# Optimization experiments

Measured on AMD Instinct MI355X. Metric: run time of the kernel, lower is better.

## Reference

```python
import jax, jax.numpy as jnp
import numpy as np

B, S, D, T = 64, 512, 768, 64


def setup_inputs() -> dict:
    key = jax.random.key(0)
    k1, k2, k3 = jax.random.split(key, 3)
    x = jax.random.normal(k1, (B, S, D), dtype=jnp.float32)
    W = jax.random.normal(k2, (T, D), dtype=jnp.float32) * 0.02
    b = jnp.zeros((T,), dtype=jnp.float32)
    transitions = jax.random.uniform(k3, (T, T), dtype=jnp.float32, minval=-0.1, maxval=0.1)
    return {"x": x, "W": W, "b": b, "transitions": transitions}


def reference(x, W, b, transitions):
    # emissions: [B,S,T] -> [S,B,T]
    em = jnp.einsum('bsd,td->bst', x, W) + b
    em = em.transpose(1, 0, 2)

    # Viterbi forward: max-plus scan over time, collecting argmax backpointers
    def step(score, em_t):
        # score: [B,T] (prev tag), em_t: [B,T] (cur tag)
        s = score[:, :, None] + transitions[None, :, :] + em_t[:, None, :]  # [B,Tprev,Tcur]
        return jnp.max(s, axis=1), jnp.argmax(s, axis=1)

    final_score, history = jax.lax.scan(step, em[0], em[1:])  # history: [S-1,B,T]

    # Backtrack (vectorized over batch) with a reverse scan
    best = jnp.argmax(final_score, axis=-1)  # [B]

    def back(nxt, idx_t):
        prev = jnp.take_along_axis(idx_t, nxt[:, None], axis=1)[:, 0]  # [B]
        return prev, prev

    _, prev_tags = jax.lax.scan(back, best, history, reverse=True)  # [S-1,B], tags for t=0..S-2
    tags = jnp.concatenate([prev_tags, best[None, :]], axis=0)  # [S,B]
    return tags.T.astype(jnp.int32)  # [B,S]
```

## Files before the change

kernel.cpp:

```cpp
#include <hip/hip_runtime.h>

#define SS 512
#define DD 768
#define TT 64

typedef __attribute__((ext_vector_type(2))) float f32x2;

__device__ __forceinline__ f32x2 vmax2(f32x2 a, f32x2 b) {
    return __builtin_elementwise_max(a, b);
}

__global__ __launch_bounds__(256) void emis_gemm(
    const float* __restrict__ X, const float* __restrict__ W,
    const float* __restrict__ bias, float* __restrict__ em)
{
    __shared__ __align__(16) float Xs[16][68];
    __shared__ __align__(16) float Ws[16][68];

    const int tid = threadIdx.x;
    const int m0  = blockIdx.x * 64;
    const int tm  = tid >> 4;
    const int tn  = tid & 15;
    const int lr  = tid >> 2;
    const int lk  = tid & 3;

    float acc[4][4];
#pragma unroll
    for (int i = 0; i < 4; i++)
#pragma unroll
        for (int j = 0; j < 4; j++) acc[i][j] = 0.f;

    float4 xr, wr;
    xr = *(const float4*)&X[(size_t)(m0 + lr) * DD + lk * 4];
    wr = *(const float4*)&W[(size_t)lr * DD + lk * 4];

    for (int t = 0; t < 48; t++) {
        Xs[lk * 4 + 0][lr] = xr.x;  Xs[lk * 4 + 1][lr] = xr.y;
        Xs[lk * 4 + 2][lr] = xr.z;  Xs[lk * 4 + 3][lr] = xr.w;
        Ws[lk * 4 + 0][lr] = wr.x;  Ws[lk * 4 + 1][lr] = wr.y;
        Ws[lk * 4 + 2][lr] = wr.z;  Ws[lk * 4 + 3][lr] = wr.w;
        __syncthreads();

        if (t < 47) {
            const int k0 = (t + 1) * 16;
            xr = *(const float4*)&X[(size_t)(m0 + lr) * DD + k0 + lk * 4];
            wr = *(const float4*)&W[(size_t)lr * DD + k0 + lk * 4];
        }

#pragma unroll
        for (int k = 0; k < 16; k++) {
            float a[4], bv[4];
            *(float4*)&a[0]  = *(const float4*)&Xs[k][tm * 4];
            *(float4*)&bv[0] = *(const float4*)&Ws[k][tn * 4];
#pragma unroll
            for (int i = 0; i < 4; i++)
#pragma unroll
                for (int j = 0; j < 4; j++)
                    acc[i][j] = fmaf(a[i], bv[j], acc[i][j]);
        }
        __syncthreads();
    }

    const float4 bv4 = *(const float4*)&bias[tn * 4];
#pragma unroll
    for (int i = 0; i < 4; i++) {
        const size_t row = (size_t)(m0 + tm * 4 + i);
        float4 o;
        o.x = acc[i][0] + bv4.x;  o.y = acc[i][1] + bv4.y;
        o.z = acc[i][2] + bv4.z;  o.w = acc[i][3] + bv4.w;
        *(float4*)&em[row * TT + tn * 4] = o;
    }
}

__global__ __launch_bounds__(64)
__attribute__((amdgpu_waves_per_eu(1, 1)))
void viterbi_fwd(
    const float* __restrict__ em, const float* __restrict__ trans,
    float* __restrict__ scoreHist, int* __restrict__ bestTag)
{
    __shared__ __align__(16) float sc_lds[TT];
    __shared__ __align__(16) float tr_lds[4096];

    const int b    = blockIdx.x;
    const int lane = threadIdx.x;
    const float* emb = em + (size_t)b * SS * TT;
    float* sh = scoreHist + (size_t)b * SS * TT;

    {
        float4* dst = (float4*)tr_lds;
        const float4* src = (const float4*)trans;
#pragma unroll
        for (int i = 0; i < 16; i++) dst[lane + i * 64] = src[lane + i * 64];
    }
    __syncthreads();

    f32x2 tpk[32];
#pragma unroll
    for (int j = 0; j < 32; j++) {
        tpk[j].x = tr_lds[(2 * j) * TT + lane];
        tpk[j].y = tr_lds[(2 * j + 1) * TT + lane];
    }

    const float em0 = emb[lane];
    sc_lds[lane] = em0;
    sh[lane] = em0;
    float sc = em0;

    float er0 = emb[1 * TT + lane];
    float er1 = emb[2 * TT + lane];
    float er2 = emb[3 * TT + lane];
    float er3 = emb[4 * TT + lane];

    float4 sq[16];
    {
        const float4* sb = (const float4*)sc_lds;
#pragma unroll
        for (int i = 0; i < 16; i++) sq[i] = sb[i];
    }

    auto step = [&](int s, float em_v) {
        const f32x2* sq2 = (const f32x2*)sq;
        f32x2 pk[32];
#pragma unroll
        for (int j = 0; j < 32; j++) pk[j] = sq2[j] + tpk[j];

#pragma unroll
        for (int m = 16; m >= 1; m >>= 1)
#pragma unroll
            for (int j = 0; j < 16; j++) {
                if (j < m) pk[j] = vmax2(pk[j], pk[j + m]);
            }
        sc = fmaxf(pk[0].x, pk[0].y) + em_v;

        sc_lds[lane] = sc;
        {
            const float4* sb = (const float4*)sc_lds;
#pragma unroll
            for (int i = 0; i < 16; i++) sq[i] = sb[i];
        }
        sh[s * TT + lane] = sc;
    };

    for (int sb = 1; sb <= 505; sb += 4) {
        step(sb + 0, er0);  er0 = emb[(sb + 4) * TT + lane];
        step(sb + 1, er1);  er1 = emb[(sb + 5) * TT + lane];
        step(sb + 2, er2);  er2 = emb[(sb + 6) * TT + lane];
        step(sb + 3, er3);  er3 = emb[((sb + 7) <= 511 ? (sb + 7) : 511) * TT + lane];
    }
    step(509, er0);
    step(510, er1);
    step(511, er2);

    float fv = sc;
    int   fa = lane;
#pragma unroll
    for (int m = 1; m <= 32; m <<= 1) {
        const float vo = __shfl_xor(fv, m, 64);
        const int   ao = __shfl_xor(fa, m, 64);
        if (vo > fv || (vo == fv && ao < fa)) { fv = vo; fa = ao; }
    }
    if (lane == 0) bestTag[b] = fa;
}

__global__ __launch_bounds__(256) void bp_kernel(
    const float* __restrict__ scoreHist, const float* __restrict__ em,
    const float* __restrict__ trans, unsigned char* __restrict__ hist8)
{
    __shared__ __align__(16) float tr_lds[4096];
    const int tid = threadIdx.x;
    {
        const float4* src = (const float4*)trans;
        float4* dst = (float4*)tr_lds;
        for (int i = tid; i < 1024; i += 256) dst[i] = src[i];
    }
    __syncthreads();

    const int wv   = tid >> 6;
    const int lane = tid & 63;
    const int g    = blockIdx.x * 4 + wv;
    const int b    = g / 511;
    const int s    = 1 + (g % 511);

    const f32x2* sb2 = (const f32x2*)(scoreHist + ((size_t)b * SS + (s - 1)) * TT);
    const float em_v = em[((size_t)b * SS + s) * TT + lane];
    const float sh_v = scoreHist[((size_t)b * SS + s) * TT + lane];

    f32x2 tpk[32];
#pragma unroll
    for (int j = 0; j < 32; j++) {
        tpk[j].x = tr_lds[(2 * j) * TT + lane];
        tpk[j].y = tr_lds[(2 * j + 1) * TT + lane];
    }

    f32x2 em2; em2.x = em_v; em2.y = em_v;
    f32x2 v2[32];
#pragma unroll
    for (int j = 0; j < 32; j++) {
        f32x2 cand = sb2[j] + tpk[j];
        v2[j] = cand + em2;
    }

    int idx = 63;
#pragma unroll
    for (int j = 31; j >= 0; j--) {
        idx = (v2[j].y == sh_v) ? 2 * j + 1 : idx;
        idx = (v2[j].x == sh_v) ? 2 * j     : idx;
    }

    hist8[((size_t)b * SS + s) * TT + lane] = (unsigned char)idx;
}

__global__ __launch_bounds__(64) void backtrack(
    const unsigned char* __restrict__ hist8, const int* __restrict__ bestTag,
    int* __restrict__ out)
{
    __shared__ int tags[SS];

    const int b    = blockIdx.x;
    const int lane = threadIdx.x;
    const unsigned char* h8 = hist8 + (size_t)b * SS * TT;

    int tag = bestTag[b];
    if (lane == 0) tags[511] = tag;

    int r0 = h8[511 * TT + lane];
    int r1 = h8[510 * TT + lane];
    int r2 = h8[509 * TT + lane];
    int r3 = h8[508 * TT + lane];

    for (int sb = 511; sb >= 11; sb -= 4) {
        tag = __builtin_amdgcn_readlane(r0, tag);
        if (lane == 0) tags[sb - 1] = tag;
        r0 = h8[(sb - 4) * TT + lane];
        tag = __builtin_amdgcn_readlane(r1, tag);
        if (lane == 0) tags[sb - 2] = tag;
        r1 = h8[(sb - 5) * TT + lane];
        tag = __builtin_amdgcn_readlane(r2, tag);
        if (lane == 0) tags[sb - 3] = tag;
        r2 = h8[(sb - 6) * TT + lane];
        tag = __builtin_amdgcn_readlane(r3, tag);
        if (lane == 0) tags[sb - 4] = tag;
        r3 = h8[(sb - 7) * TT + lane];
    }
    tag = __builtin_amdgcn_readlane(r0, tag);  if (lane == 0) tags[6] = tag;
    tag = __builtin_amdgcn_readlane(r1, tag);  if (lane == 0) tags[5] = tag;
    tag = __builtin_amdgcn_readlane(r2, tag);  if (lane == 0) tags[4] = tag;
    tag = __builtin_amdgcn_readlane(r3, tag);  if (lane == 0) tags[3] = tag;
    int q0 = h8[3 * TT + lane];
    int q1 = h8[2 * TT + lane];
    int q2 = h8[1 * TT + lane];
    tag = __builtin_amdgcn_readlane(q0, tag);  if (lane == 0) tags[2] = tag;
    tag = __builtin_amdgcn_readlane(q1, tag);  if (lane == 0) tags[1] = tag;
    tag = __builtin_amdgcn_readlane(q2, tag);  if (lane == 0) tags[0] = tag;

    __syncthreads();
#pragma unroll
    for (int s = 0; s < 8; s++)
        out[(size_t)b * SS + s * 64 + lane] = tags[s * 64 + lane];
}

extern "C" void kernel_launch(void* const* d_in, const int* in_sizes, int n_in,
                              void* d_out, int out_size, void* d_ws, size_t ws_size,
                              hipStream_t stream)
{
    const float* X     = (const float*)d_in[0];
    const float* W     = (const float*)d_in[1];
    const float* bias  = (const float*)d_in[2];
    const float* trans = (const float*)d_in[3];
    int* out = (int*)d_out;

    char* ws = (char*)d_ws;
    float*         em        = (float*)ws;
    float*         scoreHist = (float*)(ws + 8388608);
    unsigned char* hist8     = (unsigned char*)(ws + 16777216);
    int*           bestTag   = (int*)(ws + 18874368);

    emis_gemm<<<dim3(512), dim3(256), 0, stream>>>(X, W, bias, em);
    viterbi_fwd<<<dim3(64), dim3(64), 0, stream>>>(em, trans, scoreHist, bestTag);
    bp_kernel<<<dim3(8176), dim3(256), 0, stream>>>(scoreHist, em, trans, hist8);
    backtrack<<<dim3(64), dim3(64), 0, stream>>>(hist8, bestTag, out);
}
```

Before: 227.4 us.

## Fuse emission GEMM into Viterbi kernel with producer waves double-buffering chunks

Merges the emission GEMM and the Viterbi forward scan into one kernel of 64 blocks, one per batch element. Four producer waves compute 64-row emission chunks into a double-buffered LDS tile while a fifth wave runs the serial max-plus recurrence on the previous chunk. This removes a kernel launch and the serial wave's global-memory emission reads, and hides the GEMM behind the recurrence. The cost is that the GEMM now runs on only 64 CUs, and the producer waves share a CU with the latency-critical scan wave.

```diff
diff --git a/kernel.cpp b/kernel.cpp
--- a/kernel.cpp
+++ b/kernel.cpp
@@ -10,156 +10,171 @@
     return __builtin_elementwise_max(a, b);
 }
 
-__global__ __launch_bounds__(256) void emis_gemm(
+__global__ __launch_bounds__(320)
+__attribute__((amdgpu_waves_per_eu(1, 2)))
+void fused_gemm_viterbi(
     const float* __restrict__ X, const float* __restrict__ W,
-    const float* __restrict__ bias, float* __restrict__ em)
-{
-    __shared__ __align__(16) float Xs[16][68];
-    __shared__ __align__(16) float Ws[16][68];
-
-    const int tid = threadIdx.x;
-    const int m0  = blockIdx.x * 64;
-    const int tm  = tid >> 4;
-    const int tn  = tid & 15;
-    const int lr  = tid >> 2;
-    const int lk  = tid & 3;
-
-    float acc[4][4];
-#pragma unroll
-    for (int i = 0; i < 4; i++)
-#pragma unroll
-        for (int j = 0; j < 4; j++) acc[i][j] = 0.f;
-
-    float4 xr, wr;
-    xr = *(const float4*)&X[(size_t)(m0 + lr) * DD + lk * 4];
-    wr = *(const float4*)&W[(size_t)lr * DD + lk * 4];
-
-    for (int t = 0; t < 48; t++) {
-        Xs[lk * 4 + 0][lr] = xr.x;  Xs[lk * 4 + 1][lr] = xr.y;
-        Xs[lk * 4 + 2][lr] = xr.z;  Xs[lk * 4 + 3][lr] = xr.w;
-        Ws[lk * 4 + 0][lr] = wr.x;  Ws[lk * 4 + 1][lr] = wr.y;
-        Ws[lk * 4 + 2][lr] = wr.z;  Ws[lk * 4 + 3][lr] = wr.w;
-        __syncthreads();
-
-        if (t < 47) {
-            const int k0 = (t + 1) * 16;
-            xr = *(const float4*)&X[(size_t)(m0 + lr) * DD + k0 + lk * 4];
-            wr = *(const float4*)&W[(size_t)lr * DD + k0 + lk * 4];
-        }
-
-#pragma unroll
-        for (int k = 0; k < 16; k++) {
-            float a[4], bv[4];
-            *(float4*)&a[0]  = *(const float4*)&Xs[k][tm * 4];
-            *(float4*)&bv[0] = *(const float4*)&Ws[k][tn * 4];
-#pragma unroll
-            for (int i = 0; i < 4; i++)
-#pragma unroll
-                for (int j = 0; j < 4; j++)
-                    acc[i][j] = fmaf(a[i], bv[j], acc[i][j]);
-        }
-        __syncthreads();
-    }
-
-    const float4 bv4 = *(const float4*)&bias[tn * 4];
-#pragma unroll
-    for (int i = 0; i < 4; i++) {
-        const size_t row = (size_t)(m0 + tm * 4 + i);
-        float4 o;
-        o.x = acc[i][0] + bv4.x;  o.y = acc[i][1] + bv4.y;
-        o.z = acc[i][2] + bv4.z;  o.w = acc[i][3] + bv4.w;
-        *(float4*)&em[row * TT + tn * 4] = o;
-    }
-}
-
-__global__ __launch_bounds__(64)
-__attribute__((amdgpu_waves_per_eu(1, 1)))
-void viterbi_fwd(
-    const float* __restrict__ em, const float* __restrict__ trans,
-    float* __restrict__ scoreHist, int* __restrict__ bestTag)
-{
+    const float* __restrict__ bias, const float* __restrict__ trans,
+    float* __restrict__ em, float* __restrict__ scoreHist,
+    int* __restrict__ bestTag)
+{
+    __shared__ __align__(16) float em_lds[2][64][TT];
+    __shared__ __align__(16) float tr_lds[4096];
     __shared__ __align__(16) float sc_lds[TT];
-    __shared__ __align__(16) float tr_lds[4096];
+    __shared__ __align__(16) float Xs[4][16][20];
+    __shared__ __align__(16) float Ws[4][16][64];
 
     const int b    = blockIdx.x;
-    const int lane = threadIdx.x;
-    const float* emb = em + (size_t)b * SS * TT;
-    float* sh = scoreHist + (size_t)b * SS * TT;
-
-    {
+    const int tid  = threadIdx.x;
+    const int wid  = tid >> 6;
+    const int lane = tid & 63;
+
+    float* emg = em + (size_t)b * SS * TT;
+    float* sh  = scoreHist + (size_t)b * SS * TT;
+
+    const int rgrp = lane >> 4;
+    const int cgrp = lane & 15;
+    const int xrow = lane >> 2;
+    const int xkq  = lane & 3;
+    float4 bv4;
+    if (wid < 4) bv4 = *(const float4*)&bias[cgrp * 4];
+
+    auto produce = [&](int ct, int nbuf) {
+        const float4* X4 = (const float4*)X;
+        const float4* W4 = (const float4*)W;
+        const int rowbase = b * SS + ct * 64 + wid * 16;
+
+        float acc[4][4];
+#pragma unroll
+        for (int i = 0; i < 4; i++)
+#pragma unroll
+            for (int j = 0; j < 4; j++) acc[i][j] = 0.f;
+
+        float4 xr = X4[(size_t)(rowbase + xrow) * 192 + xkq];
+        float4 w0 = W4[(size_t)lane * 192 + 0];
+        float4 w1 = W4[(size_t)lane * 192 + 1];
+        float4 w2 = W4[(size_t)lane * 192 + 2];
+        float4 w3 = W4[(size_t)lane * 192 + 3];
+
+        for (int kt = 0; kt < 48; kt++) {
+            Xs[wid][xkq * 4 + 0][xrow] = xr.x;
+            Xs[wid][xkq * 4 + 1][xrow] = xr.y;
+            Xs[wid][xkq * 4 + 2][xrow] = xr.z;
+            Xs[wid][xkq * 4 + 3][xrow] = xr.w;
+            Ws[wid][ 0][lane] = w0.x;  Ws[wid][ 1][lane] = w0.y;
+            Ws[wid][ 2][lane] = w0.z;  Ws[wid][ 3][lane] = w0.w;
+            Ws[wid][ 4][lane] = w1.x;  Ws[wid][ 5][lane] = w1.y;
+            Ws[wid][ 6][lane] = w1.z;  Ws[wid][ 7][lane] = w1.w;
+            Ws[wid][ 8][lane] = w2.x;  Ws[wid][ 9][lane] = w2.y;
+            Ws[wid][10][lane] = w2.z;  Ws[wid][11][lane] = w2.w;
+            Ws[wid][12][lane] = w3.x;  Ws[wid][13][lane] = w3.y;
+            Ws[wid][14][lane] = w3.z;  Ws[wid][15][lane] = w3.w;
+
+            if (kt < 47) {
+                xr = X4[(size_t)(rowbase + xrow) * 192 + (kt + 1) * 4 + xkq];
+                w0 = W4[(size_t)lane * 192 + (kt + 1) * 4 + 0];
+                w1 = W4[(size_t)lane * 192 + (kt + 1) * 4 + 1];
+                w2 = W4[(size_t)lane * 192 + (kt + 1) * 4 + 2];
+                w3 = W4[(size_t)lane * 192 + (kt + 1) * 4 + 3];
+            }
+
+#pragma unroll
+            for (int k = 0; k < 16; k++) {
+                float a[4], bvv[4];
+                *(float4*)&a[0]   = *(const float4*)&Xs[wid][k][rgrp * 4];
+                *(float4*)&bvv[0] = *(const float4*)&Ws[wid][k][cgrp * 4];
+#pragma unroll
+                for (int i = 0; i < 4; i++)
+#pragma unroll
+                    for (int j = 0; j < 4; j++)
+                        acc[i][j] = fmaf(a[i], bvv[j], acc[i][j]);
+            }
+        }
+
+#pragma unroll
+        for (int i = 0; i < 4; i++) {
+            const int rl = wid * 16 + rgrp * 4 + i;
+            float4 o;
+            o.x = acc[i][0] + bv4.x;  o.y = acc[i][1] + bv4.y;
+            o.z = acc[i][2] + bv4.z;  o.w = acc[i][3] + bv4.w;
+            *(float4*)&em_lds[nbuf][rl][cgrp * 4] = o;
+            *(float4*)&emg[(size_t)(ct * 64 + rl) * TT + cgrp * 4] = o;
+        }
+    };
+
+    f32x2 tpk[32];
+    if (wid == 4) {
         float4* dst = (float4*)tr_lds;
         const float4* src = (const float4*)trans;
 #pragma unroll
         for (int i = 0; i < 16; i++) dst[lane + i * 64] = src[lane + i * 64];
+#pragma unroll
+        for (int j = 0; j < 32; j++) {
+            tpk[j].x = tr_lds[(2 * j) * TT + lane];
+            tpk[j].y = tr_lds[(2 * j + 1) * TT + lane];
+        }
+    } else {
+        produce(0, 0);
     }
     __syncthreads();
 
-    f32x2 tpk[32];
-#pragma unroll
-    for (int j = 0; j < 32; j++) {
-        tpk[j].x = tr_lds[(2 * j) * TT + lane];
-        tpk[j].y = tr_lds[(2 * j + 1) * TT + lane];
-    }
-
-    const float em0 = emb[lane];
-    sc_lds[lane] = em0;
-    sh[lane] = em0;
-    float sc = em0;
-
-    float er0 = emb[1 * TT + lane];
-    float er1 = emb[2 * TT + lane];
-    float er2 = emb[3 * TT + lane];
-    float er3 = emb[4 * TT + lane];
-
+    float sc = 0.f;
     float4 sq[16];
-    {
+    if (wid == 4) {
+        sc = em_lds[0][0][lane];
+        sc_lds[lane] = sc;
+        sh[lane] = sc;
         const float4* sb = (const float4*)sc_lds;
 #pragma unroll
         for (int i = 0; i < 16; i++) sq[i] = sb[i];
     }
 
-    auto step = [&](int s, float em_v) {
-        const f32x2* sq2 = (const f32x2*)sq;
-        f32x2 pk[32];
-#pragma unroll
-        for (int j = 0; j < 32; j++) pk[j] = sq2[j] + tpk[j];
-
-#pragma unroll
-        for (int m = 16; m >= 1; m >>= 1)
-#pragma unroll
-            for (int j = 0; j < 16; j++) {
-                if (j < m) pk[j] = vmax2(pk[j], pk[j + m]);
+    int buf = 0;
+    for (int cn = 0; cn < 8; cn++) {
+        if (wid == 4) {
+            const int s0 = cn * 64;
+            const int sb_ = (cn == 0) ? 1 : s0;
+#pragma unroll 4
+            for (int s = sb_; s < s0 + 64; s++) {
+                const float em_v = em_lds[buf][s - s0][lane];
+                const f32x2* sq2 = (const f32x2*)sq;
+                f32x2 pk[32];
+#pragma unroll
+                for (int j = 0; j < 32; j++) pk[j] = sq2[j] + tpk[j];
+#pragma unroll
+                for (int m = 16; m >= 1; m >>= 1)
+#pragma unroll
+                    for (int j = 0; j < 16; j++) {
+                        if (j < m) pk[j] = vmax2(pk[j], pk[j + m]);
+                    }
+                sc = fmaxf(pk[0].x, pk[0].y) + em_v;
+
+                sc_lds[lane] = sc;
+                {
+                    const float4* sb = (const float4*)sc_lds;
+#pragma unroll
+                    for (int i = 0; i < 16; i++) sq[i] = sb[i];
+                }
+                sh[(size_t)s * TT + lane] = sc;
             }
-        sc = fmaxf(pk[0].x, pk[0].y) + em_v;
-
-        sc_lds[lane] = sc;
-        {
-            const float4* sb = (const float4*)sc_lds;
-#pragma unroll
-            for (int i = 0; i < 16; i++) sq[i] = sb[i];
-        }
-        sh[s * TT + lane] = sc;
-    };
-
-    for (int sb = 1; sb <= 505; sb += 4) {
-        step(sb + 0, er0);  er0 = emb[(sb + 4) * TT + lane];
-        step(sb + 1, er1);  er1 = emb[(sb + 5) * TT + lane];
-        step(sb + 2, er2);  er2 = emb[(sb + 6) * TT + lane];
-        step(sb + 3, er3);  er3 = emb[((sb + 7) <= 511 ? (sb + 7) : 511) * TT + lane];
-    }
-    step(509, er0);
-    step(510, er1);
-    step(511, er2);
-
-    float fv = sc;
-    int   fa = lane;
-#pragma unroll
-    for (int m = 1; m <= 32; m <<= 1) {
-        const float vo = __shfl_xor(fv, m, 64);
-        const int   ao = __shfl_xor(fa, m, 64);
-        if (vo > fv || (vo == fv && ao < fa)) { fv = vo; fa = ao; }
-    }
-    if (lane == 0) bestTag[b] = fa;
+        } else if (cn < 7) {
+            produce(cn + 1, buf ^ 1);
+        }
+        __syncthreads();
+        buf ^= 1;
+    }
+
+    if (wid == 4) {
+        float fv = sc;
+        int   fa = lane;
+#pragma unroll
+        for (int m = 1; m <= 32; m <<= 1) {
+            const float vo = __shfl_xor(fv, m, 64);
+            const int   ao = __shfl_xor(fa, m, 64);
+            if (vo > fv || (vo == fv && ao < fa)) { fv = vo; fa = ao; }
+        }
+        if (lane == 0) bestTag[b] = fa;
+    }
 }
 
 __global__ __launch_bounds__(256) void bp_kernel(
@@ -275,8 +290,8 @@
     unsigned char* hist8     = (unsigned char*)(ws + 16777216);
     int*           bestTag   = (int*)(ws + 18874368);
 
-    emis_gemm<<<dim3(512), dim3(256), 0, stream>>>(X, W, bias, em);
-    viterbi_fwd<<<dim3(64), dim3(64), 0, stream>>>(em, trans, scoreHist, bestTag);
+    fused_gemm_viterbi<<<dim3(64), dim3(320), 0, stream>>>(
+        X, W, bias, trans, em, scoreHist, bestTag);
     bp_kernel<<<dim3(8176), dim3(256), 0, stream>>>(scoreHist, em, trans, hist8);
     backtrack<<<dim3(64), dim3(64), 0, stream>>>(hist8, bestTag, out);
 }
```

Result: slower. 545.1 us (+139.7%).

## Fuse backpointer recovery into Viterbi forward kernel with LDS double-buffered score history

Applied to the files above, without the earlier changes.

Merges the forward scan and backpointer kernels into one 320-thread block per batch. Wave 0 runs the serial max-plus recurrence and writes 64-step score chunks into a double-buffered LDS history. Four helper waves meanwhile recompute argmax backpointers for the previous chunk and write hist8. This removes the global scoreHist round trip and a kernel launch, overlapping backpointer work with the serial scan. The cost is a block-wide barrier every 64 steps, and the helper waves compete with the critical-path wave for issue slots.

```diff
diff --git a/kernel.cpp b/kernel.cpp
--- a/kernel.cpp
+++ b/kernel.cpp
@@ -72,21 +72,24 @@
     }
 }
 
-__global__ __launch_bounds__(64)
-__attribute__((amdgpu_waves_per_eu(1, 1)))
-void viterbi_fwd(
+__global__ __launch_bounds__(320)
+__attribute__((amdgpu_waves_per_eu(1, 2)))
+void viterbi_fused(
     const float* __restrict__ em, const float* __restrict__ trans,
-    float* __restrict__ scoreHist, int* __restrict__ bestTag)
-{
+    unsigned char* __restrict__ hist8, int* __restrict__ bestTag)
+{
+    __shared__ __align__(16) float tr_lds[4096];
     __shared__ __align__(16) float sc_lds[TT];
-    __shared__ __align__(16) float tr_lds[4096];
+    __shared__ __align__(16) float shist[2][65][TT];
 
     const int b    = blockIdx.x;
-    const int lane = threadIdx.x;
+    const int tid  = threadIdx.x;
+    const int wid  = tid >> 6;
+    const int lane = tid & 63;
     const float* emb = em + (size_t)b * SS * TT;
-    float* sh = scoreHist + (size_t)b * SS * TT;
-
-    {
+    unsigned char* hb = hist8 + (size_t)b * SS * TT;
+
+    if (wid == 0) {
         float4* dst = (float4*)tr_lds;
         const float4* src = (const float4*)trans;
 #pragma unroll
@@ -101,29 +104,29 @@
         tpk[j].y = tr_lds[(2 * j + 1) * TT + lane];
     }
 
-    const float em0 = emb[lane];
-    sc_lds[lane] = em0;
-    sh[lane] = em0;
-    float sc = em0;
-
-    float er0 = emb[1 * TT + lane];
-    float er1 = emb[2 * TT + lane];
-    float er2 = emb[3 * TT + lane];
-    float er3 = emb[4 * TT + lane];
-
+    float sc = 0.f;
     float4 sq[16];
-    {
+    float er0 = 0.f, er1 = 0.f, er2 = 0.f, er3 = 0.f;
+    if (wid == 0) {
+        const float em0 = emb[lane];
+        sc = em0;
+        sc_lds[lane] = em0;
+        shist[0][1][lane] = em0;
+        er0 = emb[1 * TT + lane];
+        er1 = emb[2 * TT + lane];
+        er2 = emb[3 * TT + lane];
+        er3 = emb[4 * TT + lane];
         const float4* sb = (const float4*)sc_lds;
 #pragma unroll
         for (int i = 0; i < 16; i++) sq[i] = sb[i];
     }
+    __syncthreads();
 
     auto step = [&](int s, float em_v) {
         const f32x2* sq2 = (const f32x2*)sq;
         f32x2 pk[32];
 #pragma unroll
         for (int j = 0; j < 32; j++) pk[j] = sq2[j] + tpk[j];
-
 #pragma unroll
         for (int m = 16; m >= 1; m >>= 1)
 #pragma unroll
@@ -138,76 +141,80 @@
 #pragma unroll
             for (int i = 0; i < 16; i++) sq[i] = sb[i];
         }
-        sh[s * TT + lane] = sc;
+        shist[(s >> 6) & 1][(s & 63) + 1][lane] = sc;
     };
 
-    for (int sb = 1; sb <= 505; sb += 4) {
-        step(sb + 0, er0);  er0 = emb[(sb + 4) * TT + lane];
-        step(sb + 1, er1);  er1 = emb[(sb + 5) * TT + lane];
-        step(sb + 2, er2);  er2 = emb[(sb + 6) * TT + lane];
-        step(sb + 3, er3);  er3 = emb[((sb + 7) <= 511 ? (sb + 7) : 511) * TT + lane];
-    }
-    step(509, er0);
-    step(510, er1);
-    step(511, er2);
-
-    float fv = sc;
-    int   fa = lane;
-#pragma unroll
-    for (int m = 1; m <= 32; m <<= 1) {
-        const float vo = __shfl_xor(fv, m, 64);
-        const int   ao = __shfl_xor(fa, m, 64);
-        if (vo > fv || (vo == fv && ao < fa)) { fv = vo; fa = ao; }
-    }
-    if (lane == 0) bestTag[b] = fa;
-}
-
-__global__ __launch_bounds__(256) void bp_kernel(
-    const float* __restrict__ scoreHist, const float* __restrict__ em,
-    const float* __restrict__ trans, unsigned char* __restrict__ hist8)
-{
-    __shared__ __align__(16) float tr_lds[4096];
-    const int tid = threadIdx.x;
-    {
-        const float4* src = (const float4*)trans;
-        float4* dst = (float4*)tr_lds;
-        for (int i = tid; i < 1024; i += 256) dst[i] = src[i];
-    }
-    __syncthreads();
-
-    const int wv   = tid >> 6;
-    const int lane = tid & 63;
-    const int g    = blockIdx.x * 4 + wv;
-    const int b    = g / 511;
-    const int s    = 1 + (g % 511);
-
-    const f32x2* sb2 = (const f32x2*)(scoreHist + ((size_t)b * SS + (s - 1)) * TT);
-    const float em_v = em[((size_t)b * SS + s) * TT + lane];
-    const float sh_v = scoreHist[((size_t)b * SS + s) * TT + lane];
-
-    f32x2 tpk[32];
-#pragma unroll
-    for (int j = 0; j < 32; j++) {
-        tpk[j].x = tr_lds[(2 * j) * TT + lane];
-        tpk[j].y = tr_lds[(2 * j + 1) * TT + lane];
-    }
-
-    f32x2 em2; em2.x = em_v; em2.y = em_v;
-    f32x2 v2[32];
-#pragma unroll
-    for (int j = 0; j < 32; j++) {
-        f32x2 cand = sb2[j] + tpk[j];
-        v2[j] = cand + em2;
-    }
-
-    int idx = 63;
-#pragma unroll
-    for (int j = 31; j >= 0; j--) {
-        idx = (v2[j].y == sh_v) ? 2 * j + 1 : idx;
-        idx = (v2[j].x == sh_v) ? 2 * j     : idx;
-    }
-
-    hist8[((size_t)b * SS + s) * TT + lane] = (unsigned char)idx;
+    auto bp_chunk = [&](int cc) {
+        const int buf = cc & 1;
+        for (int k = 0; k < 16; ++k) {
+            const int sl = (wid - 1) + 4 * k;
+            const int s  = cc * 64 + sl;
+            if (s == 0) continue;
+            const f32x2* sb2 = (const f32x2*)&shist[buf][sl][0];
+            const float em_v = emb[(size_t)s * TT + lane];
+            const float sh_v = shist[buf][sl + 1][lane];
+            f32x2 em2; em2.x = em_v; em2.y = em_v;
+            f32x2 v2[32];
+#pragma unroll
+            for (int j = 0; j < 32; j++) {
+                f32x2 cand = sb2[j] + tpk[j];
+                v2[j] = cand + em2;
+            }
+            int idx = 63;
+#pragma unroll
+            for (int j = 31; j >= 0; j--) {
+                idx = (v2[j].y == sh_v) ? 2 * j + 1 : idx;
+                idx = (v2[j].x == sh_v) ? 2 * j     : idx;
+            }
+            hb[(size_t)s * TT + lane] = (unsigned char)idx;
+        }
+    };
+
+    for (int c = 0; c < 8; ++c) {
+        if (wid == 0) {
+            if (c > 0) shist[c & 1][0][lane] = sc;
+            if (c == 0) {
+                step(1, er0);  er0 = emb[5 * TT + lane];
+                step(2, er1);  er1 = emb[6 * TT + lane];
+                step(3, er2);  er2 = emb[7 * TT + lane];
+                for (int sb = 4; sb <= 60; sb += 4) {
+                    step(sb + 0, er3);  er3 = emb[(sb + 4) * TT + lane];
+                    step(sb + 1, er0);  er0 = emb[(sb + 5) * TT + lane];
+                    step(sb + 2, er1);  er1 = emb[(sb + 6) * TT + lane];
+                    step(sb + 3, er2);  er2 = emb[(sb + 7) * TT + lane];
+                }
+            } else {
+                for (int q = 0; q < 16; ++q) {
+                    const int sb = c * 64 + q * 4;
+                    const int p4 = (sb + 4 <= 511) ? sb + 4 : 511;
+                    const int p5 = (sb + 5 <= 511) ? sb + 5 : 511;
+                    const int p6 = (sb + 6 <= 511) ? sb + 6 : 511;
+                    const int p7 = (sb + 7 <= 511) ? sb + 7 : 511;
+                    step(sb + 0, er3);  er3 = emb[p4 * TT + lane];
+                    step(sb + 1, er0);  er0 = emb[p5 * TT + lane];
+                    step(sb + 2, er1);  er1 = emb[p6 * TT + lane];
+                    step(sb + 3, er2);  er2 = emb[p7 * TT + lane];
+                }
+            }
+        } else if (c > 0) {
+            bp_chunk(c - 1);
+        }
+        __syncthreads();
+    }
+
+    if (wid == 0) {
+        float fv = sc;
+        int   fa = lane;
+#pragma unroll
+        for (int m = 1; m <= 32; m <<= 1) {
+            const float vo = __shfl_xor(fv, m, 64);
+            const int   ao = __shfl_xor(fa, m, 64);
+            if (vo > fv || (vo == fv && ao < fa)) { fv = vo; fa = ao; }
+        }
+        if (lane == 0) bestTag[b] = fa;
+    } else {
+        bp_chunk(7);
+    }
 }
 
 __global__ __launch_bounds__(64) void backtrack(
@@ -270,13 +277,11 @@
     int* out = (int*)d_out;
 
     char* ws = (char*)d_ws;
-    float*         em        = (float*)ws;
-    float*         scoreHist = (float*)(ws + 8388608);
-    unsigned char* hist8     = (unsigned char*)(ws + 16777216);
-    int*           bestTag   = (int*)(ws + 18874368);
+    float*         em      = (float*)ws;
+    unsigned char* hist8   = (unsigned char*)(ws + 8388608);
+    int*           bestTag = (int*)(ws + 10485760);
 
     emis_gemm<<<dim3(512), dim3(256), 0, stream>>>(X, W, bias, em);
-    viterbi_fwd<<<dim3(64), dim3(64), 0, stream>>>(em, trans, scoreHist, bestTag);
-    bp_kernel<<<dim3(8176), dim3(256), 0, stream>>>(scoreHist, em, trans, hist8);
+    viterbi_fused<<<dim3(64), dim3(320), 0, stream>>>(em, trans, hist8, bestTag);
     backtrack<<<dim3(64), dim3(64), 0, stream>>>(hist8, bestTag, out);
 }
```

New measurement: 246.4 us. 8.4% more time.

## Replace LDS-tiled emission GEMM with per-wave register GEMM over transposed W

Applied to the files above, without the earlier changes.

Adds a small kernel that transposes W into workspace so each lane owns one tag column. The emission GEMM drops its shared-memory tiles and barriers: each wave computes 16 rows by 64 tags, prefetching W values into registers and reading X rows with uniform float4 loads. This removes LDS traffic and syncs. In exchange, each wave reads 16 X rows straight from global memory through the cache, and an extra kernel launch is added.

```diff
diff --git a/kernel.cpp b/kernel.cpp
--- a/kernel.cpp
+++ b/kernel.cpp
@@ -10,66 +10,53 @@
     return __builtin_elementwise_max(a, b);
 }
 
+__global__ __launch_bounds__(256) void transpose_w(
+    const float* __restrict__ W, float* __restrict__ WT)
+{
+    const int idx = blockIdx.x * 256 + threadIdx.x;
+    WT[idx] = W[(idx & 63) * DD + (idx >> 6)];
+}
+
 __global__ __launch_bounds__(256) void emis_gemm(
-    const float* __restrict__ X, const float* __restrict__ W,
+    const float* __restrict__ X, const float* __restrict__ WT,
     const float* __restrict__ bias, float* __restrict__ em)
 {
-    __shared__ __align__(16) float Xs[16][68];
-    __shared__ __align__(16) float Ws[16][68];
-
-    const int tid = threadIdx.x;
-    const int m0  = blockIdx.x * 64;
-    const int tm  = tid >> 4;
-    const int tn  = tid & 15;
-    const int lr  = tid >> 2;
-    const int lk  = tid & 3;
-
-    float acc[4][4];
-#pragma unroll
-    for (int i = 0; i < 4; i++)
-#pragma unroll
-        for (int j = 0; j < 4; j++) acc[i][j] = 0.f;
-
-    float4 xr, wr;
-    xr = *(const float4*)&X[(size_t)(m0 + lr) * DD + lk * 4];
-    wr = *(const float4*)&W[(size_t)lr * DD + lk * 4];
-
-    for (int t = 0; t < 48; t++) {
-        Xs[lk * 4 + 0][lr] = xr.x;  Xs[lk * 4 + 1][lr] = xr.y;
-        Xs[lk * 4 + 2][lr] = xr.z;  Xs[lk * 4 + 3][lr] = xr.w;
-        Ws[lk * 4 + 0][lr] = wr.x;  Ws[lk * 4 + 1][lr] = wr.y;
-        Ws[lk * 4 + 2][lr] = wr.z;  Ws[lk * 4 + 3][lr] = wr.w;
-        __syncthreads();
-
-        if (t < 47) {
-            const int k0 = (t + 1) * 16;
-            xr = *(const float4*)&X[(size_t)(m0 + lr) * DD + k0 + lk * 4];
-            wr = *(const float4*)&W[(size_t)lr * DD + k0 + lk * 4];
+    const int wave = blockIdx.x * 4 + (threadIdx.x >> 6);
+    const int lane = threadIdx.x & 63;
+    const int row0 = wave * 16;
+
+    float acc[16];
+#pragma unroll
+    for (int r = 0; r < 16; r++) acc[r] = 0.f;
+
+    float wt[8];
+#pragma unroll
+    for (int j = 0; j < 8; j++) wt[j] = WT[j * TT + lane];
+
+    for (int k = 0; k < DD; k += 8) {
+        float w0 = wt[0], w1 = wt[1], w2 = wt[2], w3 = wt[3];
+        float w4 = wt[4], w5 = wt[5], w6 = wt[6], w7 = wt[7];
+        if (k + 8 < DD) {
+#pragma unroll
+            for (int j = 0; j < 8; j++) wt[j] = WT[(k + 8 + j) * TT + lane];
         }
-
-#pragma unroll
-        for (int k = 0; k < 16; k++) {
-            float a[4], bv[4];
-            *(float4*)&a[0]  = *(const float4*)&Xs[k][tm * 4];
-            *(float4*)&bv[0] = *(const float4*)&Ws[k][tn * 4];
-#pragma unroll
-            for (int i = 0; i < 4; i++)
-#pragma unroll
-                for (int j = 0; j < 4; j++)
-                    acc[i][j] = fmaf(a[i], bv[j], acc[i][j]);
+#pragma unroll
+        for (int r = 0; r < 16; r++) {
+            const float4 x0 = *(const float4*)&X[(size_t)(row0 + r) * DD + k];
+            const float4 x1 = *(const float4*)&X[(size_t)(row0 + r) * DD + k + 4];
+            float a = acc[r];
+            a = fmaf(x0.x, w0, a);  a = fmaf(x0.y, w1, a);
+            a = fmaf(x0.z, w2, a);  a = fmaf(x0.w, w3, a);
+            a = fmaf(x1.x, w4, a);  a = fmaf(x1.y, w5, a);
+            a = fmaf(x1.z, w6, a);  a = fmaf(x1.w, w7, a);
+            acc[r] = a;
         }
-        __syncthreads();
-    }
-
-    const float4 bv4 = *(const float4*)&bias[tn * 4];
-#pragma unroll
-    for (int i = 0; i < 4; i++) {
-        const size_t row = (size_t)(m0 + tm * 4 + i);
-        float4 o;
-        o.x = acc[i][0] + bv4.x;  o.y = acc[i][1] + bv4.y;
-        o.z = acc[i][2] + bv4.z;  o.w = acc[i][3] + bv4.w;
-        *(float4*)&em[row * TT + tn * 4] = o;
-    }
+    }
+
+    const float bv = bias[lane];
+#pragma unroll
+    for (int r = 0; r < 16; r++)
+        em[(size_t)(row0 + r) * TT + lane] = acc[r] + bv;
 }
 
 __global__ __launch_bounds__(64)
@@ -274,8 +261,10 @@
     float*         scoreHist = (float*)(ws + 8388608);
     unsigned char* hist8     = (unsigned char*)(ws + 16777216);
     int*           bestTag   = (int*)(ws + 18874368);
-
-    emis_gemm<<<dim3(512), dim3(256), 0, stream>>>(X, W, bias, em);
+    float*         WT        = (float*)(ws + 18874624);
+
+    transpose_w<<<dim3(192), dim3(256), 0, stream>>>(W, WT);
+    emis_gemm<<<dim3(512), dim3(256), 0, stream>>>(X, WT, bias, em);
     viterbi_fwd<<<dim3(64), dim3(64), 0, stream>>>(em, trans, scoreHist, bestTag);
     bp_kernel<<<dim3(8176), dim3(256), 0, stream>>>(scoreHist, em, trans, hist8);
     backtrack<<<dim3(64), dim3(64), 0, stream>>>(hist8, bestTag, out);
```

After: 371.6 us. 1.63x slower.
